# Kernel optimization log

Measured on AMD Instinct MI355X. Metric: run time of the kernel, lower is better.

The kernel has to match this reference:

```python
import jax, jax.numpy as jnp
import numpy as np

N_CLASSES = 512


def setup_inputs() -> dict:
    key = jax.random.key(0)
    k1, k2 = jax.random.split(key)
    B, T, C, V = 16, 2048, 1, 256
    x0 = jax.random.normal(k1, (B, T, C, V), dtype=jnp.float32)
    # nn.Parameter(torch.randn(...) * embedding_scale) with embedding_scale = 0.001
    embedding0 = jax.random.normal(k2, (C, N_CLASSES, V), dtype=jnp.float32) * 0.001
    return {"x0": x0, "embedding0": embedding0}


def reference(x0, embedding0):
    # normalize=False path: x = x0, embedding = embedding0
    B, T, C, V = x0.shape
    K = embedding0.shape[1]
    x = x0
    emb = embedding0

    # Nearest-codebook search. Original materializes (chunk, C, K, V) diffs and
    # (same argmin) to avoid the huge broadcasted intermediate.
    x1 = x.reshape(B * T, C, V)                      # (N, C, V)
    x_sq = jnp.sum(x1 * x1, axis=-1)[:, :, None]     # (N, C, 1)
    e_sq = jnp.sum(emb * emb, axis=-1)[None]         # (1, C, K)
    cross = jnp.einsum('ncv,ckv->nck', x1, emb)      # (N, C, K)
    d2 = x_sq - 2.0 * cross + e_sq                   # (N, C, K)
    index = jnp.argmin(d2, axis=2)                   # (N, C) int

    # entropy of code usage (histogram over all selected indices)
    hist = jnp.bincount(index.reshape(-1), length=K).astype(jnp.float32)
    prob = hist / jnp.float32(index.shape[0])        # divide by N = len(index)
    entropy = -jnp.sum(jnp.where(hist > 0, prob * jnp.log(prob), 0.0))

    # gather codebook vectors
    offset = jnp.arange(C, dtype=index.dtype) * K    # (C,)
    index1 = (index + offset[None, :]).reshape(-1)   # (N*C,)
    output = emb.reshape(C * K, V)[index1].reshape(B, T, C, V)

    # straight-through output + VQ / commitment losses
    out0 = jax.lax.stop_gradient(output - x) + x
    out1 = jnp.sum((jax.lax.stop_gradient(x) - output) ** 2, axis=3)   # (B,T,C)
    out2 = jnp.sum((x - jax.lax.stop_gradient(output)) ** 2, axis=3) \
         + jnp.sum((x - x0) ** 2, axis=3)                              # zero term when normalize=False
    return out0, out1, out2, entropy
```

## Files before the change

kernel.cpp:

```cpp
#include <hip/hip_runtime.h>
#include <math.h>

#define NV 256
#define NK 512
#define BM 64
#define WM 16
#define TSH 4096
#define TGSH 16384
#define NPH 8

typedef unsigned long long ull;
typedef unsigned short u16;
typedef unsigned int u32;
using short8  = __attribute__((ext_vector_type(8))) short;
using floatx4 = __attribute__((ext_vector_type(4))) float;

__device__ __forceinline__ u16 f2bf(float f) {
    unsigned int u = __float_as_uint(f);
    u += 0x7fffu + ((u >> 16) & 1u);
    return (u16)(u >> 16);
}
__device__ __forceinline__ float bf2f(u16 h) {
    return __uint_as_float(((unsigned int)h) << 16);
}
__device__ __forceinline__ floatx4 mfma16(short8 a, short8 b, floatx4 c) {
    return __builtin_amdgcn_mfma_f32_16x16x32_bf16(a, b, c, 0, 0, 0);
}
__device__ __forceinline__ void gload_lds16(const u16* g, u16* l) {
    __builtin_amdgcn_global_load_lds(
        (const __attribute__((address_space(1))) void*)g,
        (__attribute__((address_space(3))) void*)l, 16, 0, 0);
}

__global__ __launch_bounds__(256) void vq_prepcvt(const float* __restrict__ emb,
                                                  float* __restrict__ esq1,
                                                  u16* __restrict__ ehws,
                                                  int* __restrict__ hist) {
    const int t = threadIdx.x;
    const int lane = t & 63;
    const int code = blockIdx.x * 4 + (t >> 6);
    const int nt = code >> 4, c = code & 15;
    const float4 v = *(const float4*)(emb + (size_t)code * NV + lane * 4);
    ushort4 h;
    h.x = f2bf(v.x);
    h.y = f2bf(v.y);
    h.z = f2bf(v.z);
    h.w = f2bf(v.w);
    const size_t base = (size_t)nt * TSH + (size_t)(lane >> 1) * 128 + c * 8 + (lane & 1) * 4;
    *(ushort4*)(ehws + base) = h;
    float s = v.x * v.x + v.y * v.y + v.z * v.z + v.w * v.w;
#pragma unroll
    for (int m = 1; m <= 32; m <<= 1) s += __shfl_xor(s, m, 64);
    if (lane == 0) esq1[code] = s + 2.0f;
    const int g = blockIdx.x * 256 + t;
    if (g < NK) hist[g] = 0;
}

__global__ __launch_bounds__(256, 2) void vq_main(
    const float* __restrict__ x,
    const float* __restrict__ emb,
    const u16* __restrict__ ehws,
    const float* __restrict__ esq1,
    int* __restrict__ hist,
    float* __restrict__ out0,
    float* __restrict__ out1,
    float* __restrict__ out2) {
    __shared__ u16 lds_b[2 * TGSH];
    __shared__ float esq_lds[NK];
    __shared__ int idx_lds[BM];

    const int t = threadIdx.x;
    const int wid = t >> 6;
    const int lane = t & 63;
    const int lr = lane & 15;
    const int lg = lane >> 4;
    const size_t n0w = (size_t)blockIdx.x * BM + (size_t)wid * WM;

#define STAGE(B, P) do {                                                    \
        const u16* gs = ehws + (size_t)(P) * TGSH + wid * 4096 + lane * 8;  \
        u16* lb = &lds_b[(B) * TGSH + wid * 4096];                          \
        gload_lds16(gs,        lb);                                         \
        gload_lds16(gs +  512, lb +  512);                                  \
        gload_lds16(gs + 1024, lb + 1024);                                  \
        gload_lds16(gs + 1536, lb + 1536);                                  \
        gload_lds16(gs + 2048, lb + 2048);                                  \
        gload_lds16(gs + 2560, lb + 2560);                                  \
        gload_lds16(gs + 3072, lb + 3072);                                  \
        gload_lds16(gs + 3584, lb + 3584);                                  \
    } while (0)

    STAGE(0, 0);

    esq_lds[t] = esq1[t];
    esq_lds[t + 256] = esq1[t + 256];

    short8 ah[8], al[8];
#pragma unroll
    for (int ks = 0; ks < 8; ++ks) {
        const float* p = x + (n0w + lr) * NV + ks * 32 + lg * 8;
        float4 u0 = *(const float4*)p;
        float4 u1 = *(const float4*)(p + 4);
        float f[8] = {u0.x, u0.y, u0.z, u0.w, u1.x, u1.y, u1.z, u1.w};
        short8 h, l;
#pragma unroll
        for (int j = 0; j < 8; ++j) {
            u16 hb = f2bf(f[j]);
            h[j] = (short)hb;
            l[j] = (short)f2bf(f[j] - bf2f(hb));
        }
        ah[ks] = h;
        al[ks] = l;
    }

    u32 rmin[4];
#pragma unroll
    for (int j = 0; j < 4; ++j) rmin[j] = 0xffffffffu;

#pragma unroll 2
    for (int p = 0; p < NPH; ++p) {
        const int pn = (p + 1 < NPH) ? (p + 1) : (NPH - 1);
        STAGE((p + 1) & 1, pn);
        asm volatile("s_waitcnt vmcnt(8) lgkmcnt(0)" ::: "memory");
        __builtin_amdgcn_s_barrier();
        asm volatile("" ::: "memory");

        const u16* gb = &lds_b[(p & 1) * TGSH];
        __builtin_amdgcn_s_setprio(1);
#pragma unroll
        for (int tt = 0; tt < 4; ++tt) {
            const int nt = 4 * p + tt;
            const u16* bb = gb + tt * TSH + lane * 8;
            floatx4 acc = {0.f, 0.f, 0.f, 0.f};
#pragma unroll
            for (int ks = 0; ks < 8; ++ks) {
                short8 bh = *(const short8*)(bb + ks * 512);
                acc = mfma16(ah[ks], bh, acc);
            }
            const float evq = esq_lds[nt * 16 + lr];
            const u32 code = (u32)(nt * 16 + lr);
#pragma unroll
            for (int j = 0; j < 4; ++j) {
                float d = fmaf(-2.0f, acc[j], evq);
                u32 key = (__float_as_uint(d) & 0xfffffe00u) | code;
                rmin[j] = min(rmin[j], key);
            }
        }
        __builtin_amdgcn_s_setprio(0);

        asm volatile("s_waitcnt lgkmcnt(0)" ::: "memory");
        __builtin_amdgcn_s_barrier();
        asm volatile("" ::: "memory");
    }
#undef STAGE

#pragma unroll
    for (int j = 0; j < 4; ++j) {
#pragma unroll
        for (int m = 1; m <= 8; m <<= 1) {
            u32 v = (u32)__shfl_xor((int)rmin[j], m, 64);
            rmin[j] = min(rmin[j], v);
        }
    }
    if (lr == 0) {
#pragma unroll
        for (int j = 0; j < 4; ++j) {
            int i0 = (int)(rmin[j] & 511u);
            idx_lds[wid * WM + lg * 4 + j] = i0;
            atomicAdd(&hist[i0], 1);
        }
    }
    __syncthreads();

    const int idx = idx_lds[wid * WM + lr];
    float s0 = 0.0f;
#pragma unroll
    for (int ks = 0; ks < 8; ++ks) {
        const float* ep = emb + (size_t)idx * NV + ks * 32 + lg * 8;
        float4 e0 = *(const float4*)ep;
        float4 e1 = *(const float4*)(ep + 4);
        float ee[8] = {e0.x, e0.y, e0.z, e0.w, e1.x, e1.y, e1.z, e1.w};
        float ov[8];
#pragma unroll
        for (int j = 0; j < 8; ++j) {
            float xv = bf2f((u16)ah[ks][j]) + bf2f((u16)al[ks][j]);
            ov[j] = (ee[j] - xv) + xv;
            float d = xv - ee[j];
            s0 += d * d;
        }
        float* dst = out0 + (n0w + lr) * NV + ks * 32 + lg * 8;
        *(float4*)dst       = *(float4*)&ov[0];
        *(float4*)(dst + 4) = *(float4*)&ov[4];
    }
    s0 += __shfl_xor(s0, 16, 64);
    s0 += __shfl_xor(s0, 32, 64);
    if (lg == 0) {
        out1[n0w + lr] = s0;
        out2[n0w + lr] = s0;
    }
}

__global__ __launch_bounds__(256) void vq_entropy(const int* __restrict__ hist,
                                                  float* __restrict__ out_ent,
                                                  int n_rows) {
    __shared__ float sdata[256];
    int t = threadIdx.x;
    float local = 0.0f;
    float invn = 1.0f / (float)n_rows;
    for (int k = t; k < NK; k += 256) {
        int h = hist[k];
        if (h > 0) {
            float p = (float)h * invn;
            local += p * logf(p);
        }
    }
    sdata[t] = local;
    __syncthreads();
    for (int s = 128; s >= 1; s >>= 1) {
        if (t < s) sdata[t] += sdata[t + s];
        __syncthreads();
    }
    if (t == 0) *out_ent = -sdata[0];
}

extern "C" void kernel_launch(void* const* d_in, const int* in_sizes, int n_in,
                              void* d_out, int out_size, void* d_ws, size_t ws_size,
                              hipStream_t stream) {
    const float* x   = (const float*)d_in[0];
    const float* emb = (const float*)d_in[1];

    const int n_rows = in_sizes[0] / NV;

    float* out0 = (float*)d_out;
    float* out1 = out0 + (size_t)n_rows * NV;
    float* out2 = out1 + n_rows;
    float* ent  = out2 + n_rows;

    float* esq1 = (float*)d_ws;
    int* hist   = (int*)(esq1 + NK);
    u16* ehws   = (u16*)(hist + NK);

    vq_prepcvt<<<NK / 4, 256, 0, stream>>>(emb, esq1, ehws, hist);
    vq_main<<<n_rows / BM, 256, 0, stream>>>(x, emb, ehws, esq1, hist,
                                             out0, out1, out2);
    vq_entropy<<<1, 256, 0, stream>>>(hist, ent, n_rows);
}
```

Baseline: 52.77 us.

## Stream codebook tiles from global into registers and fuse entropy via last-block

Drops the LDS double-buffered codebook staging and its barriers. Each wave now loads bf16 codebook tiles straight from global/L2 into registers, triple-buffered, and splits each tile's MFMA chain into two independent accumulators. The entropy kernel is folded into the main kernel through an atomic counter, so the last block computes entropy and one launch disappears. The trade-off is more global/L2 traffic per wave, since loads are no longer shared across waves, plus higher register pressure.

```diff
diff --git a/kernel.cpp b/kernel.cpp
--- a/kernel.cpp
+++ b/kernel.cpp
@@ -6,10 +6,7 @@
 #define BM 64
 #define WM 16
 #define TSH 4096
-#define TGSH 16384
-#define NPH 8
-
-typedef unsigned long long ull;
+
 typedef unsigned short u16;
 typedef unsigned int u32;
 using short8  = __attribute__((ext_vector_type(8))) short;
@@ -26,16 +23,12 @@
 __device__ __forceinline__ floatx4 mfma16(short8 a, short8 b, floatx4 c) {
     return __builtin_amdgcn_mfma_f32_16x16x32_bf16(a, b, c, 0, 0, 0);
 }
-__device__ __forceinline__ void gload_lds16(const u16* g, u16* l) {
-    __builtin_amdgcn_global_load_lds(
-        (const __attribute__((address_space(1))) void*)g,
-        (__attribute__((address_space(3))) void*)l, 16, 0, 0);
-}
 
 __global__ __launch_bounds__(256) void vq_prepcvt(const float* __restrict__ emb,
                                                   float* __restrict__ esq1,
                                                   u16* __restrict__ ehws,
-                                                  int* __restrict__ hist) {
+                                                  int* __restrict__ hist,
+                                                  int* __restrict__ counter) {
     const int t = threadIdx.x;
     const int lane = t & 63;
     const int code = blockIdx.x * 4 + (t >> 6);
@@ -54,7 +47,30 @@
     if (lane == 0) esq1[code] = s + 2.0f;
     const int g = blockIdx.x * 256 + t;
     if (g < NK) hist[g] = 0;
-}
+    if (g == 0) *counter = 0;
+}
+
+#define LOADT(R, T) do {                                                      \
+    const u16* gp = bb + (size_t)(T) * TSH;                                   \
+    _Pragma("unroll")                                                         \
+    for (int ks = 0; ks < 8; ++ks) R[ks] = *(const short8*)(gp + ks * 512);   \
+} while (0)
+
+#define COMPUTE(R, T) do {                                                    \
+    floatx4 ae = {0.f, 0.f, 0.f, 0.f}, ao = {0.f, 0.f, 0.f, 0.f};             \
+    ae = mfma16(ah[0], R[0], ae);  ao = mfma16(ah[1], R[1], ao);              \
+    ae = mfma16(ah[2], R[2], ae);  ao = mfma16(ah[3], R[3], ao);              \
+    ae = mfma16(ah[4], R[4], ae);  ao = mfma16(ah[5], R[5], ao);              \
+    ae = mfma16(ah[6], R[6], ae);  ao = mfma16(ah[7], R[7], ao);              \
+    const float evq = esq_lds[(T) * 16 + lr];                                 \
+    const u32 code = (u32)((T) * 16 + lr);                                    \
+    _Pragma("unroll")                                                         \
+    for (int j = 0; j < 4; ++j) {                                             \
+        float d = fmaf(-2.0f, ae[j] + ao[j], evq);               \
+        u32 key = (__float_as_uint(d) & 0xfffffe00u) | code;                  \
+        rmin[j] = min(rmin[j], key);                                          \
+    }                                                                         \
+} while (0)
 
 __global__ __launch_bounds__(256, 2) void vq_main(
     const float* __restrict__ x,
@@ -62,12 +78,15 @@
     const u16* __restrict__ ehws,
     const float* __restrict__ esq1,
     int* __restrict__ hist,
+    int* __restrict__ counter,
     float* __restrict__ out0,
     float* __restrict__ out1,
-    float* __restrict__ out2) {
-    __shared__ u16 lds_b[2 * TGSH];
+    float* __restrict__ out2,
+    float* __restrict__ ent,
+    int n_rows) {
     __shared__ float esq_lds[NK];
     __shared__ int idx_lds[BM];
+    __shared__ int s_last;
 
     const int t = threadIdx.x;
     const int wid = t >> 6;
@@ -75,21 +94,11 @@
     const int lr = lane & 15;
     const int lg = lane >> 4;
     const size_t n0w = (size_t)blockIdx.x * BM + (size_t)wid * WM;
-
-#define STAGE(B, P) do {                                                    \
-        const u16* gs = ehws + (size_t)(P) * TGSH + wid * 4096 + lane * 8;  \
-        u16* lb = &lds_b[(B) * TGSH + wid * 4096];                          \
-        gload_lds16(gs,        lb);                                         \
-        gload_lds16(gs +  512, lb +  512);                                  \
-        gload_lds16(gs + 1024, lb + 1024);                                  \
-        gload_lds16(gs + 1536, lb + 1536);                                  \
-        gload_lds16(gs + 2048, lb + 2048);                                  \
-        gload_lds16(gs + 2560, lb + 2560);                                  \
-        gload_lds16(gs + 3072, lb + 3072);                                  \
-        gload_lds16(gs + 3584, lb + 3584);                                  \
-    } while (0)
-
-    STAGE(0, 0);
+    const u16* bb = ehws + lane * 8;
+
+    short8 bA[8], bB[8], bC[8];
+    LOADT(bA, 0);
+    LOADT(bB, 1);
 
     esq_lds[t] = esq1[t];
     esq_lds[t + 256] = esq1[t + 256];
@@ -116,42 +125,18 @@
 #pragma unroll
     for (int j = 0; j < 4; ++j) rmin[j] = 0xffffffffu;
 
-#pragma unroll 2
-    for (int p = 0; p < NPH; ++p) {
-        const int pn = (p + 1 < NPH) ? (p + 1) : (NPH - 1);
-        STAGE((p + 1) & 1, pn);
-        asm volatile("s_waitcnt vmcnt(8) lgkmcnt(0)" ::: "memory");
-        __builtin_amdgcn_s_barrier();
-        asm volatile("" ::: "memory");
-
-        const u16* gb = &lds_b[(p & 1) * TGSH];
-        __builtin_amdgcn_s_setprio(1);
-#pragma unroll
-        for (int tt = 0; tt < 4; ++tt) {
-            const int nt = 4 * p + tt;
-            const u16* bb = gb + tt * TSH + lane * 8;
-            floatx4 acc = {0.f, 0.f, 0.f, 0.f};
-#pragma unroll
-            for (int ks = 0; ks < 8; ++ks) {
-                short8 bh = *(const short8*)(bb + ks * 512);
-                acc = mfma16(ah[ks], bh, acc);
-            }
-            const float evq = esq_lds[nt * 16 + lr];
-            const u32 code = (u32)(nt * 16 + lr);
-#pragma unroll
-            for (int j = 0; j < 4; ++j) {
-                float d = fmaf(-2.0f, acc[j], evq);
-                u32 key = (__float_as_uint(d) & 0xfffffe00u) | code;
-                rmin[j] = min(rmin[j], key);
-            }
-        }
-        __builtin_amdgcn_s_setprio(0);
-
-        asm volatile("s_waitcnt lgkmcnt(0)" ::: "memory");
-        __builtin_amdgcn_s_barrier();
-        asm volatile("" ::: "memory");
-    }
-#undef STAGE
+    __syncthreads();
+
+    for (int tb = 0; tb < 30; tb += 3) {
+        LOADT(bC, tb + 2);
+        COMPUTE(bA, tb);
+        LOADT(bA, tb + 3);
+        COMPUTE(bB, tb + 1);
+        LOADT(bB, tb + 4);
+        COMPUTE(bC, tb + 2);
+    }
+    COMPUTE(bA, 30);
+    COMPUTE(bB, 31);
 
 #pragma unroll
     for (int j = 0; j < 4; ++j) {
@@ -170,6 +155,11 @@
         }
     }
     __syncthreads();
+
+    if (t == 0) {
+        __threadfence();
+        s_last = (atomicAdd(counter, 1) == (int)gridDim.x - 1);
+    }
 
     const int idx = idx_lds[wid * WM + lr];
     float s0 = 0.0f;
@@ -197,29 +187,26 @@
         out1[n0w + lr] = s0;
         out2[n0w + lr] = s0;
     }
-}
-
-__global__ __launch_bounds__(256) void vq_entropy(const int* __restrict__ hist,
-                                                  float* __restrict__ out_ent,
-                                                  int n_rows) {
-    __shared__ float sdata[256];
-    int t = threadIdx.x;
-    float local = 0.0f;
-    float invn = 1.0f / (float)n_rows;
-    for (int k = t; k < NK; k += 256) {
-        int h = hist[k];
-        if (h > 0) {
-            float p = (float)h * invn;
-            local += p * logf(p);
-        }
-    }
-    sdata[t] = local;
+
     __syncthreads();
-    for (int s = 128; s >= 1; s >>= 1) {
-        if (t < s) sdata[t] += sdata[t + s];
+    if (s_last) {
+        float local = 0.0f;
+        const float invn = 1.0f / (float)n_rows;
+        for (int k = t; k < NK; k += 256) {
+            int h = atomicAdd(&hist[k], 0);
+            if (h > 0) {
+                float p = (float)h * invn;
+                local += p * logf(p);
+            }
+        }
+        esq_lds[t] = local;
         __syncthreads();
-    }
-    if (t == 0) *out_ent = -sdata[0];
+        for (int s = 128; s >= 1; s >>= 1) {
+            if (t < s) esq_lds[t] += esq_lds[t + s];
+            __syncthreads();
+        }
+        if (t == 0) *ent = -esq_lds[0];
+    }
 }
 
 extern "C" void kernel_launch(void* const* d_in, const int* in_sizes, int n_in,
@@ -235,12 +222,12 @@
     float* out2 = out1 + n_rows;
     float* ent  = out2 + n_rows;
 
-    float* esq1 = (float*)d_ws;
-    int* hist   = (int*)(esq1 + NK);
-    u16* ehws   = (u16*)(hist + NK);
-
-    vq_prepcvt<<<NK / 4, 256, 0, stream>>>(emb, esq1, ehws, hist);
-    vq_main<<<n_rows / BM, 256, 0, stream>>>(x, emb, ehws, esq1, hist,
-                                             out0, out1, out2);
-    vq_entropy<<<1, 256, 0, stream>>>(hist, ent, n_rows);
-}
+    float* esq1   = (float*)d_ws;
+    int* hist     = (int*)(esq1 + NK);
+    int* counter  = hist + NK;
+    u16* ehws     = (u16*)(counter + 4);
+
+    vq_prepcvt<<<NK / 4, 256, 0, stream>>>(emb, esq1, ehws, hist, counter);
+    vq_main<<<n_rows / BM, 256, 0, stream>>>(x, emb, ehws, esq1, hist, counter,
+                                             out0, out1, out2, ent, n_rows);
+}
```

New measurement: 74.74 us. +41.6%, slower.
